# Kernel optimization log

Measured on AMD Instinct MI355X. Metric: run time of the kernel, lower is better.

Reference implementation:

```python
import jax, jax.numpy as jnp
import numpy as np

N_NODES = 100000
N_EDGES = 1600000
N_GRAPHS = 1024
N_FEAT = 128
HID = 64
N_CLASSES = 16
N_CENT = 3  # centroids per class


def setup_inputs() -> dict:
    key = jax.random.key(0)
    ks = jax.random.split(key, 8)
    x = jax.random.normal(ks[0], (N_NODES, N_FEAT), dtype=jnp.float32)
    edge_index = jax.random.randint(ks[1], (2, N_EDGES), 0, N_NODES, dtype=jnp.int64)
    batch = jnp.sort(jax.random.randint(ks[2], (N_NODES,), 0, N_GRAPHS, dtype=jnp.int64))
    s = 1.0 / np.sqrt(N_FEAT)
    W1 = jax.random.normal(ks[3], (N_FEAT, HID), dtype=jnp.float32) * s
    W2 = jax.random.normal(ks[4], (HID, HID), dtype=jnp.float32) * (1.0 / np.sqrt(HID))
    W3 = jax.random.normal(ks[5], (HID, HID), dtype=jnp.float32) * (1.0 / np.sqrt(HID))
    b1 = jnp.zeros((HID,), jnp.float32)
    b2 = jnp.zeros((HID,), jnp.float32)
    b3 = jnp.zeros((HID,), jnp.float32)
    centroids = jax.random.normal(ks[6], (N_CLASSES * N_CENT, HID), dtype=jnp.float32)
    reject_bias = jnp.zeros((1,), jnp.float32)
    return {"x": x, "edge_index": edge_index, "batch": batch,
            "W1": W1, "b1": b1, "W2": W2, "b2": b2, "W3": W3, "b3": b3,
            "centroids": centroids, "reject_bias": reject_bias}


def _gcn_conv(x, W, b, src, dst, norm, n_nodes):
    # PyG GCNConv: out[dst] = sum_e norm_e * (x[src_e] @ W), + bias
    h = x @ W                      # [N, out]
    msg = h[src] * norm[:, None]   # [E+N, out] gather + scale
    out = jax.ops.segment_sum(msg, dst, num_segments=n_nodes)
    return out + b


def reference(x, edge_index, batch, W1, b1, W2, b2, W3, b3, centroids, reject_bias):
    n = x.shape[0]
    loops = jnp.arange(n, dtype=edge_index.dtype)
    src = jnp.concatenate([edge_index[0], loops])
    dst = jnp.concatenate([edge_index[1], loops])
    # symmetric normalization on A + I
    deg = jax.ops.segment_sum(jnp.ones_like(dst, dtype=x.dtype), dst, num_segments=n)
    dinv = jax.lax.rsqrt(jnp.maximum(deg, 1.0))
    norm = dinv[src] * dinv[dst]

    h = jax.nn.relu(_gcn_conv(x, W1, b1, src, dst, norm, n))  # dropout is identity at eval
    h = jax.nn.relu(_gcn_conv(h, W2, b2, src, dst, norm, n))
    h = _gcn_conv(h, W3, b3, src, dst, norm, n)

    # global mean pool over graphs in the batch
    summ = jax.ops.segment_sum(h, batch, num_segments=N_GRAPHS)          # [G, HID]
    cnt = jax.ops.segment_sum(jnp.ones((n,), h.dtype), batch, num_segments=N_GRAPHS)
    emb = summ / jnp.maximum(cnt, 1.0)[:, None]

    # centroid distance head: squared euclidean to all class centroids
    d = (jnp.sum(emb * emb, -1, keepdims=True)
         - 2.0 * emb @ centroids.T
         + jnp.sum(centroids * centroids, -1))                           # [G, 16*3]
    d_pc = jnp.min(d.reshape(-1, N_CLASSES, N_CENT), axis=-1)            # [G, 16]
    class_logits = -d_pc
    reject_logit = jnp.min(d_pc, axis=-1, keepdims=True) - reject_bias   # [G, 1]
    return jnp.concatenate([class_logits, reject_logit], axis=-1)        # [G, 17]
```

## Files before the change

kernel.cpp:

```cpp
#include <hip/hip_runtime.h>

#define HID 64
#define NCLS 16
#define NCENT 3
#define NCENTS (NCLS * NCENT)
#define BSHIFT 9
#define BINW (1 << BSHIFT)
#define NBINMAX 256
#define CHUNK 4096
#define EPT (CHUNK / 256)

static inline int ceil_div(int a, int b) { return (a + b - 1) / b; }

__device__ inline unsigned short f2bf(float f) {
    unsigned int u = __float_as_uint(f);
    return (unsigned short)((u + 0x7FFFu + ((u >> 16) & 1u)) >> 16);
}
__device__ inline float bf2f(unsigned short h) {
    return __uint_as_float(((unsigned int)h) << 16);
}


__global__ void k_count(const int* __restrict__ dst, int* __restrict__ binCnt,
                        int E, int nbins) {
    __shared__ int c[NBINMAX];
    for (int i = threadIdx.x; i < nbins; i += 256) c[i] = 0;
    __syncthreads();
    int e = blockIdx.x * CHUNK + threadIdx.x;
#pragma unroll
    for (int j = 0; j < EPT; j++, e += 256)
        if (e < E) atomicAdd(&c[dst[e] >> BSHIFT], 1);
    __syncthreads();
    for (int i = threadIdx.x; i < nbins; i += 256)
        if (c[i] > 0) atomicAdd(&binCnt[i], c[i]);
}

__global__ void k_binoff(const int* __restrict__ binCnt, int* __restrict__ binBase,
                         int nbins, int E) {
    __shared__ int ts[NBINMAX];
    int t = threadIdx.x;
    int v = (t < nbins) ? binCnt[t] : 0;
    ts[t] = v;
    __syncthreads();
    for (int off = 1; off < NBINMAX; off <<= 1) {
        int x = (t >= off) ? ts[t - off] : 0;
        __syncthreads();
        ts[t] += x;
        __syncthreads();
    }
    if (t < nbins) binBase[t] = ts[t] - v;
    if (t == 0) binBase[nbins] = E;
}

__global__ __launch_bounds__(256) void k_bin(const int* __restrict__ src,
                                             const int* __restrict__ dst,
                                             const int* __restrict__ binBase,
                                             int* __restrict__ binCur,
                                             int2* __restrict__ binned,
                                             int E, int nbins) {
    __shared__ int cnt[NBINMAX], off[NBINMAX], gbase[NBINMAX];
    __shared__ int2 stage[CHUNK];
    const int c0 = blockIdx.x * CHUNK;
    const int tid = threadIdx.x;
    cnt[tid] = 0;
    __syncthreads();
    int sv[EPT], dv[EPT];
#pragma unroll
    for (int j = 0; j < EPT; j++) {
        int e = c0 + j * 256 + tid;
        dv[j] = -1;
        if (e < E) {
            sv[j] = src[e];
            dv[j] = dst[e];
            atomicAdd(&cnt[dv[j] >> BSHIFT], 1);
        }
    }
    __syncthreads();
    off[tid] = cnt[tid];
    __syncthreads();
    for (int o = 1; o < NBINMAX; o <<= 1) {
        int x = (tid >= o) ? off[tid - o] : 0;
        __syncthreads();
        off[tid] += x;
        __syncthreads();
    }
    int excl = off[tid] - cnt[tid];
    __syncthreads();
    off[tid] = excl;
    gbase[tid] = (tid < nbins && cnt[tid] > 0) ? atomicAdd(&binCur[tid], cnt[tid]) : 0;
    cnt[tid] = 0;
    __syncthreads();
#pragma unroll
    for (int j = 0; j < EPT; j++)
        if (dv[j] >= 0) {
            int b = dv[j] >> BSHIFT;
            int pos = off[b] + atomicAdd(&cnt[b], 1);
            stage[pos] = make_int2(sv[j], dv[j]);
        }
    __syncthreads();
    int tot = min(CHUNK, E - c0);
    for (int i = tid; i < tot; i += 256) {
        int2 v = stage[i];
        int b = v.y >> BSHIFT;
        binned[binBase[b] + gbase[b] + (i - off[b])] = v;
    }
}

__global__ __launch_bounds__(256) void k_hist(const int2* __restrict__ binned,
                                              const int* __restrict__ binBase,
                                              int* __restrict__ deg, int N) {
    __shared__ int c[BINW];
    int b = blockIdx.x;
    int s = binBase[b], e = binBase[b + 1];
    int n0 = b << BSHIFT;
    for (int i = threadIdx.x; i < BINW; i += 256) c[i] = 0;
    __syncthreads();
    for (int i = s + threadIdx.x; i < e; i += 256)
        atomicAdd(&c[binned[i].y - n0], 1);
    __syncthreads();
    for (int i = threadIdx.x; i < BINW; i += 256)
        if (n0 + i < N) deg[n0 + i] = c[i];
}


__global__ void k_scan1(const int* __restrict__ deg, int* __restrict__ bsum, int N) {
    __shared__ int ts[256];
    int t = threadIdx.x;
    int base = blockIdx.x * 1024 + t * 4;
    int s = 0;
#pragma unroll
    for (int j = 0; j < 4; j++) if (base + j < N) s += deg[base + j];
    ts[t] = s;
    __syncthreads();
    for (int off = 128; off > 0; off >>= 1) {
        if (t < off) ts[t] += ts[t + off];
        __syncthreads();
    }
    if (t == 0) bsum[blockIdx.x] = ts[0];
}

__global__ void k_scan2(int* __restrict__ bsum, int B) {
    __shared__ int ts[256];
    int t = threadIdx.x;
    int v = (t < B) ? bsum[t] : 0;
    ts[t] = v;
    __syncthreads();
    for (int off = 1; off < 256; off <<= 1) {
        int x = (t >= off) ? ts[t - off] : 0;
        __syncthreads();
        ts[t] += x;
        __syncthreads();
    }
    if (t < B) bsum[t] = ts[t] - v;
}

__global__ void k_scan3(const int* __restrict__ deg, const int* __restrict__ boff,
                        int* __restrict__ rs, float* __restrict__ dinv, int N) {
    __shared__ int ts[256];
    int t = threadIdx.x;
    int base = blockIdx.x * 1024 + t * 4;
    int v[4];
    int s = 0;
#pragma unroll
    for (int j = 0; j < 4; j++) {
        v[j] = (base + j < N) ? deg[base + j] : 0;
        s += v[j];
    }
    ts[t] = s;
    __syncthreads();
    for (int off = 1; off < 256; off <<= 1) {
        int x = (t >= off) ? ts[t - off] : 0;
        __syncthreads();
        ts[t] += x;
        __syncthreads();
    }
    int run = boff[blockIdx.x] + ts[t] - s;
#pragma unroll
    for (int j = 0; j < 4; j++) {
        if (base + j < N) {
            rs[base + j] = run;
            dinv[base + j] = rsqrtf((float)(v[j] + 1));
            run += v[j];
        }
    }
}

__global__ __launch_bounds__(256) void k_fillc(const int2* __restrict__ binned,
                                               const int* __restrict__ binBase,
                                               const int* __restrict__ rs,
                                               int* __restrict__ col, int N) {
    __shared__ int cur[BINW];
    __shared__ int rsl[BINW];
    int b = blockIdx.x;
    int s = binBase[b], e = binBase[b + 1];
    int n0 = b << BSHIFT;
    for (int i = threadIdx.x; i < BINW; i += 256) {
        cur[i] = 0;
        rsl[i] = (n0 + i < N) ? rs[n0 + i] : 0;
    }
    __syncthreads();
    for (int i = s + threadIdx.x; i < e; i += 256) {
        int2 v = binned[i];
        int lo = v.y - n0;
        int pos = rsl[lo] + atomicAdd(&cur[lo], 1);
        col[pos] = v.x;
    }
}


template <int K, bool BF>
__global__ __launch_bounds__(256) void k_gemm(const void* __restrict__ Ain,
                                              const float* __restrict__ W,
                                              unsigned short* __restrict__ out, int N) {
    __shared__ float Ws[64 * HID];
    __shared__ float As[64][68];
    const int tx = threadIdx.x & 15;
    const int ty = threadIdx.x >> 4;
    const int row0 = blockIdx.x * 64;

    float acc[4][4] = {};

    for (int k0 = 0; k0 < K; k0 += 64) {
        if (k0 > 0) __syncthreads();
        for (int i = threadIdx.x; i < 64 * 16; i += 256)
            ((float4*)Ws)[i] = ((const float4*)(W + (size_t)k0 * HID))[i];
        for (int i = threadIdx.x; i < 64 * 16; i += 256) {
            int r = i >> 4, c = i & 15;
            int row = row0 + r;
            float4 v = {0.f, 0.f, 0.f, 0.f};
            if (row < N) {
                if (BF) {
                    ushort4 u = *(const ushort4*)((const unsigned short*)Ain +
                                                  (size_t)row * K + k0 + 4 * c);
                    v.x = bf2f(u.x); v.y = bf2f(u.y); v.z = bf2f(u.z); v.w = bf2f(u.w);
                } else {
                    v = *(const float4*)((const float*)Ain + (size_t)row * K + k0 + 4 * c);
                }
            }
            *(float4*)&As[r][4 * c] = v;
        }
        __syncthreads();
#pragma unroll 4
        for (int k = 0; k < 64; k++) {
            float4 w = *(const float4*)&Ws[k * HID + 4 * tx];
#pragma unroll
            for (int i = 0; i < 4; i++) {
                float a = As[4 * ty + i][k];
                acc[i][0] = fmaf(a, w.x, acc[i][0]);
                acc[i][1] = fmaf(a, w.y, acc[i][1]);
                acc[i][2] = fmaf(a, w.z, acc[i][2]);
                acc[i][3] = fmaf(a, w.w, acc[i][3]);
            }
        }
    }
#pragma unroll
    for (int i = 0; i < 4; i++) {
        int row = row0 + 4 * ty + i;
        if (row < N) {
            ushort4 v = {f2bf(acc[i][0]), f2bf(acc[i][1]), f2bf(acc[i][2]), f2bf(acc[i][3])};
            *(ushort4*)&out[(size_t)row * HID + 4 * tx] = v;
        }
    }
}


__global__ void k_agg(const unsigned short* __restrict__ tin,
                      unsigned short* __restrict__ out,
                      const int* __restrict__ rs, const int* __restrict__ deg,
                      const int* __restrict__ col,
                      const float* __restrict__ dinv, const float* __restrict__ bias,
                      int N, int relu) {
    int node = (blockIdx.x * blockDim.x + threadIdx.x) >> 4;
    int l = threadIdx.x & 15;
    if (node >= N) return;
    float di = dinv[node];
    ushort4 tb = ((const ushort4*)(tin + (size_t)node * HID))[l];
    float s2 = di * di;
    float ax = s2 * bf2f(tb.x), ay = s2 * bf2f(tb.y);
    float az = s2 * bf2f(tb.z), aw = s2 * bf2f(tb.w);

    int beg = rs[node];
    int cnt = deg[node];
    int last = beg + cnt - 1;
    for (int e = 0; e < cnt; e += 8) {
        int sv[8];
#pragma unroll
        for (int j = 0; j < 8; j++) {
            int idx = beg + e + j;
            sv[j] = col[idx < last ? idx : last];
        }
        float dvv[8];
#pragma unroll
        for (int j = 0; j < 8; j++) dvv[j] = dinv[sv[j]];
        ushort4 vv[8];
#pragma unroll
        for (int j = 0; j < 8; j++) vv[j] = ((const ushort4*)(tin + (size_t)sv[j] * HID))[l];
#pragma unroll
        for (int j = 0; j < 8; j++) {
            float w = (e + j < cnt) ? dvv[j] * di : 0.0f;
            ax = fmaf(w, bf2f(vv[j].x), ax); ay = fmaf(w, bf2f(vv[j].y), ay);
            az = fmaf(w, bf2f(vv[j].z), az); aw = fmaf(w, bf2f(vv[j].w), aw);
        }
    }
    float4 b = ((const float4*)bias)[l];
    ax += b.x; ay += b.y; az += b.z; aw += b.w;
    if (relu) {
        ax = fmaxf(ax, 0.f); ay = fmaxf(ay, 0.f);
        az = fmaxf(az, 0.f); aw = fmaxf(aw, 0.f);
    }
    ushort4 o = {f2bf(ax), f2bf(ay), f2bf(az), f2bf(aw)};
    ((ushort4*)(out + (size_t)node * HID))[l] = o;
}


__global__ void k_pool_head(const unsigned short* __restrict__ h,
                            const int* __restrict__ batch,
                            const float* __restrict__ cent, const float* __restrict__ rbias,
                            float* __restrict__ out, int N) {
    int g = blockIdx.x;
    int lo = 0, hi = N;
    while (lo < hi) { int mid = (lo + hi) >> 1; if (batch[mid] < g) lo = mid + 1; else hi = mid; }
    int s = lo;
    lo = 0; hi = N;
    while (lo < hi) { int mid = (lo + hi) >> 1; if (batch[mid] < g + 1) lo = mid + 1; else hi = mid; }
    int e = lo;

    __shared__ float part[4][HID];
    __shared__ float embS[HID];
    __shared__ float dS[NCENTS];
    __shared__ float dpcS[NCLS];

    int lane = threadIdx.x & 63, wid = threadIdx.x >> 6;
    float acc = 0.0f;
    for (int i = s + wid; i < e; i += 4) acc += bf2f(h[(size_t)i * HID + lane]);
    part[wid][lane] = acc;
    __syncthreads();
    if (wid == 0) {
        float v = part[0][lane] + part[1][lane] + part[2][lane] + part[3][lane];
        embS[lane] = v / fmaxf((float)(e - s), 1.0f);
    }
    __syncthreads();
    if (threadIdx.x < NCENTS) {
        const float* c = cent + threadIdx.x * HID;
        float d = 0.0f;
        for (int k = 0; k < HID; k++) { float df = embS[k] - c[k]; d = fmaf(df, df, d); }
        dS[threadIdx.x] = d;
    }
    __syncthreads();
    if (threadIdx.x < NCLS) {
        float m = fminf(dS[threadIdx.x * 3],
                        fminf(dS[threadIdx.x * 3 + 1], dS[threadIdx.x * 3 + 2]));
        dpcS[threadIdx.x] = m;
        out[g * (NCLS + 1) + threadIdx.x] = -m;
    }
    __syncthreads();
    if (threadIdx.x == 0) {
        float m = dpcS[0];
        for (int i = 1; i < NCLS; i++) m = fminf(m, dpcS[i]);
        out[g * (NCLS + 1) + NCLS] = m - rbias[0];
    }
}


extern "C" void kernel_launch(void* const* d_in, const int* in_sizes, int n_in,
                              void* d_out, int out_size, void* d_ws, size_t ws_size,
                              hipStream_t stream) {
    const float* x    = (const float*)d_in[0];
    const int*   ei   = (const int*)d_in[1];
    const int*   bat  = (const int*)d_in[2];
    const float* W1   = (const float*)d_in[3];
    const float* b1   = (const float*)d_in[4];
    const float* W2   = (const float*)d_in[5];
    const float* b2   = (const float*)d_in[6];
    const float* W3   = (const float*)d_in[7];
    const float* b3   = (const float*)d_in[8];
    const float* cent = (const float*)d_in[9];
    const float* rb   = (const float*)d_in[10];
    float* out = (float*)d_out;

    const int N = in_sizes[0] / 128;
    const int E = in_sizes[1] / 2;
    const int B1 = ceil_div(N, 1024);
    const int nbins = (N + BINW - 1) >> BSHIFT;

    char* p = (char*)d_ws;
    unsigned short* A  = (unsigned short*)p; p += (size_t)N * HID * 2;
    unsigned short* Bb = (unsigned short*)p; p += (size_t)N * HID * 2;
    int2*  binned = (int2*)p;  p += (size_t)E * 8;
    int*   col    = (int*)p;   p += (size_t)E * 4;
    float* dinv   = (float*)p; p += (size_t)N * 4;
    int*   rs     = (int*)p;   p += (size_t)N * 4;
    int*   deg    = (int*)p;   p += (size_t)N * 4;
    int*   bsum   = (int*)p;   p += (size_t)((B1 + 1) & ~1) * 4;
    int*   binBase= (int*)p;   p += (NBINMAX + 2) * 4;
    int*   binCnt = (int*)p;   p += NBINMAX * 4;
    int*   binCur = (int*)p;   p += NBINMAX * 4;

    hipMemsetAsync(binCnt, 0, 2 * NBINMAX * 4, stream);

    k_count<<<ceil_div(E, CHUNK), 256, 0, stream>>>(ei + E, binCnt, E, nbins);
    k_binoff<<<1, 256, 0, stream>>>(binCnt, binBase, nbins, E);
    k_bin<<<ceil_div(E, CHUNK), 256, 0, stream>>>(ei, ei + E, binBase, binCur, binned, E, nbins);
    k_hist<<<nbins, 256, 0, stream>>>(binned, binBase, deg, N);
    k_scan1<<<B1, 256, 0, stream>>>(deg, bsum, N);
    k_scan2<<<1, 256, 0, stream>>>(bsum, B1);
    k_scan3<<<B1, 256, 0, stream>>>(deg, bsum, rs, dinv, N);
    k_fillc<<<nbins, 256, 0, stream>>>(binned, binBase, rs, col, N);

    k_gemm<128, false><<<ceil_div(N, 64), 256, 0, stream>>>(x, W1, A, N);
    k_agg<<<ceil_div(N * 16, 256), 256, 0, stream>>>(A, Bb, rs, deg, col, dinv, b1, N, 1);
    k_gemm<64, true><<<ceil_div(N, 64), 256, 0, stream>>>(Bb, W2, A, N);
    k_agg<<<ceil_div(N * 16, 256), 256, 0, stream>>>(A, Bb, rs, deg, col, dinv, b2, N, 1);
    k_gemm<64, true><<<ceil_div(N, 64), 256, 0, stream>>>(Bb, W3, A, N);
    k_agg<<<ceil_div(N * 16, 256), 256, 0, stream>>>(A, Bb, rs, deg, col, dinv, b3, N, 0);

    k_pool_head<<<1024, 256, 0, stream>>>(Bb, bat, cent, rb, out, N);
}
```

Baseline: 364.0 us.

## Fuse CSR histogram, scan and fill into one kernel; widen aggregation lanes

Result: faster. 353.3 us (-2.9%).

```diff
diff --git a/kernel.cpp b/kernel.cpp
--- a/kernel.cpp
+++ b/kernel.cpp
@@ -16,9 +16,14 @@
     unsigned int u = __float_as_uint(f);
     return (unsigned short)((u + 0x7FFFu + ((u >> 16) & 1u)) >> 16);
 }
+__device__ inline unsigned int pack2bf(float lo, float hi) {
+    return (unsigned int)f2bf(lo) | ((unsigned int)f2bf(hi) << 16);
+}
 __device__ inline float bf2f(unsigned short h) {
     return __uint_as_float(((unsigned int)h) << 16);
 }
+__device__ inline float bflo(unsigned int u) { return __uint_as_float(u << 16); }
+__device__ inline float bfhi(unsigned int u) { return __uint_as_float(u & 0xFFFF0000u); }
 
 
 __global__ void k_count(const int* __restrict__ dst, int* __restrict__ binCnt,
@@ -106,44 +111,26 @@
     }
 }
 
-__global__ __launch_bounds__(256) void k_hist(const int2* __restrict__ binned,
-                                              const int* __restrict__ binBase,
-                                              int* __restrict__ deg, int N) {
+__global__ __launch_bounds__(256) void k_fillc2(const int2* __restrict__ binned,
+                                                const int* __restrict__ binBase,
+                                                int* __restrict__ col,
+                                                int* __restrict__ rs_out,
+                                                int* __restrict__ deg_out,
+                                                float* __restrict__ dinv_out, int N) {
     __shared__ int c[BINW];
+    __shared__ int rsl[BINW];
+    __shared__ int ts[256];
     int b = blockIdx.x;
     int s = binBase[b], e = binBase[b + 1];
     int n0 = b << BSHIFT;
-    for (int i = threadIdx.x; i < BINW; i += 256) c[i] = 0;
-    __syncthreads();
-    for (int i = s + threadIdx.x; i < e; i += 256)
+    int t = threadIdx.x;
+    c[2 * t] = 0; c[2 * t + 1] = 0;
+    __syncthreads();
+    for (int i = s + t; i < e; i += 256)
         atomicAdd(&c[binned[i].y - n0], 1);
     __syncthreads();
-    for (int i = threadIdx.x; i < BINW; i += 256)
-        if (n0 + i < N) deg[n0 + i] = c[i];
-}
-
-
-__global__ void k_scan1(const int* __restrict__ deg, int* __restrict__ bsum, int N) {
-    __shared__ int ts[256];
-    int t = threadIdx.x;
-    int base = blockIdx.x * 1024 + t * 4;
-    int s = 0;
-#pragma unroll
-    for (int j = 0; j < 4; j++) if (base + j < N) s += deg[base + j];
-    ts[t] = s;
-    __syncthreads();
-    for (int off = 128; off > 0; off >>= 1) {
-        if (t < off) ts[t] += ts[t + off];
-        __syncthreads();
-    }
-    if (t == 0) bsum[blockIdx.x] = ts[0];
-}
-
-__global__ void k_scan2(int* __restrict__ bsum, int B) {
-    __shared__ int ts[256];
-    int t = threadIdx.x;
-    int v = (t < B) ? bsum[t] : 0;
-    ts[t] = v;
+    int v0 = c[2 * t], v1 = c[2 * t + 1];
+    ts[t] = v0 + v1;
     __syncthreads();
     for (int off = 1; off < 256; off <<= 1) {
         int x = (t >= off) ? ts[t - off] : 0;
@@ -151,58 +138,24 @@
         ts[t] += x;
         __syncthreads();
     }
-    if (t < B) bsum[t] = ts[t] - v;
-}
-
-__global__ void k_scan3(const int* __restrict__ deg, const int* __restrict__ boff,
-                        int* __restrict__ rs, float* __restrict__ dinv, int N) {
-    __shared__ int ts[256];
-    int t = threadIdx.x;
-    int base = blockIdx.x * 1024 + t * 4;
-    int v[4];
-    int s = 0;
-#pragma unroll
-    for (int j = 0; j < 4; j++) {
-        v[j] = (base + j < N) ? deg[base + j] : 0;
-        s += v[j];
-    }
-    ts[t] = s;
-    __syncthreads();
-    for (int off = 1; off < 256; off <<= 1) {
-        int x = (t >= off) ? ts[t - off] : 0;
-        __syncthreads();
-        ts[t] += x;
-        __syncthreads();
-    }
-    int run = boff[blockIdx.x] + ts[t] - s;
-#pragma unroll
-    for (int j = 0; j < 4; j++) {
-        if (base + j < N) {
-            rs[base + j] = run;
-            dinv[base + j] = rsqrtf((float)(v[j] + 1));
-            run += v[j];
-        }
-    }
-}
-
-__global__ __launch_bounds__(256) void k_fillc(const int2* __restrict__ binned,
-                                               const int* __restrict__ binBase,
-                                               const int* __restrict__ rs,
-                                               int* __restrict__ col, int N) {
-    __shared__ int cur[BINW];
-    __shared__ int rsl[BINW];
-    int b = blockIdx.x;
-    int s = binBase[b], e = binBase[b + 1];
-    int n0 = b << BSHIFT;
-    for (int i = threadIdx.x; i < BINW; i += 256) {
-        cur[i] = 0;
-        rsl[i] = (n0 + i < N) ? rs[n0 + i] : 0;
-    }
-    __syncthreads();
-    for (int i = s + threadIdx.x; i < e; i += 256) {
+    int base = binBase[b] + ts[t] - (v0 + v1);
+    rsl[2 * t] = base;
+    rsl[2 * t + 1] = base + v0;
+    int n = n0 + 2 * t;
+    if (n < N) {
+        deg_out[n] = v0; rs_out[n] = base;
+        dinv_out[n] = rsqrtf((float)(v0 + 1));
+    }
+    if (n + 1 < N) {
+        deg_out[n + 1] = v1; rs_out[n + 1] = base + v0;
+        dinv_out[n + 1] = rsqrtf((float)(v1 + 1));
+    }
+    c[2 * t] = 0; c[2 * t + 1] = 0;
+    __syncthreads();
+    for (int i = s + t; i < e; i += 256) {
         int2 v = binned[i];
         int lo = v.y - n0;
-        int pos = rsl[lo] + atomicAdd(&cur[lo], 1);
+        int pos = rsl[lo] + atomicAdd(&c[lo], 1);
         col[pos] = v.x;
     }
 }
@@ -270,14 +223,16 @@
                       const int* __restrict__ col,
                       const float* __restrict__ dinv, const float* __restrict__ bias,
                       int N, int relu) {
-    int node = (blockIdx.x * blockDim.x + threadIdx.x) >> 4;
-    int l = threadIdx.x & 15;
+    int node = (blockIdx.x * blockDim.x + threadIdx.x) >> 3;
+    int l = threadIdx.x & 7;
     if (node >= N) return;
     float di = dinv[node];
-    ushort4 tb = ((const ushort4*)(tin + (size_t)node * HID))[l];
+    uint4 tb = ((const uint4*)(tin + (size_t)node * HID))[l];
     float s2 = di * di;
-    float ax = s2 * bf2f(tb.x), ay = s2 * bf2f(tb.y);
-    float az = s2 * bf2f(tb.z), aw = s2 * bf2f(tb.w);
+    float a0 = s2 * bflo(tb.x), a1 = s2 * bfhi(tb.x);
+    float a2 = s2 * bflo(tb.y), a3 = s2 * bfhi(tb.y);
+    float a4 = s2 * bflo(tb.z), a5 = s2 * bfhi(tb.z);
+    float a6 = s2 * bflo(tb.w), a7 = s2 * bfhi(tb.w);
 
     int beg = rs[node];
     int cnt = deg[node];
@@ -292,24 +247,30 @@
         float dvv[8];
 #pragma unroll
         for (int j = 0; j < 8; j++) dvv[j] = dinv[sv[j]];
-        ushort4 vv[8];
-#pragma unroll
-        for (int j = 0; j < 8; j++) vv[j] = ((const ushort4*)(tin + (size_t)sv[j] * HID))[l];
+        uint4 vv[8];
+#pragma unroll
+        for (int j = 0; j < 8; j++) vv[j] = ((const uint4*)(tin + (size_t)sv[j] * HID))[l];
 #pragma unroll
         for (int j = 0; j < 8; j++) {
             float w = (e + j < cnt) ? dvv[j] * di : 0.0f;
-            ax = fmaf(w, bf2f(vv[j].x), ax); ay = fmaf(w, bf2f(vv[j].y), ay);
-            az = fmaf(w, bf2f(vv[j].z), az); aw = fmaf(w, bf2f(vv[j].w), aw);
-        }
-    }
-    float4 b = ((const float4*)bias)[l];
-    ax += b.x; ay += b.y; az += b.z; aw += b.w;
+            a0 = fmaf(w, bflo(vv[j].x), a0); a1 = fmaf(w, bfhi(vv[j].x), a1);
+            a2 = fmaf(w, bflo(vv[j].y), a2); a3 = fmaf(w, bfhi(vv[j].y), a3);
+            a4 = fmaf(w, bflo(vv[j].z), a4); a5 = fmaf(w, bfhi(vv[j].z), a5);
+            a6 = fmaf(w, bflo(vv[j].w), a6); a7 = fmaf(w, bfhi(vv[j].w), a7);
+        }
+    }
+    float4 b0 = ((const float4*)bias)[2 * l];
+    float4 b1 = ((const float4*)bias)[2 * l + 1];
+    a0 += b0.x; a1 += b0.y; a2 += b0.z; a3 += b0.w;
+    a4 += b1.x; a5 += b1.y; a6 += b1.z; a7 += b1.w;
     if (relu) {
-        ax = fmaxf(ax, 0.f); ay = fmaxf(ay, 0.f);
-        az = fmaxf(az, 0.f); aw = fmaxf(aw, 0.f);
-    }
-    ushort4 o = {f2bf(ax), f2bf(ay), f2bf(az), f2bf(aw)};
-    ((ushort4*)(out + (size_t)node * HID))[l] = o;
+        a0 = fmaxf(a0, 0.f); a1 = fmaxf(a1, 0.f); a2 = fmaxf(a2, 0.f); a3 = fmaxf(a3, 0.f);
+        a4 = fmaxf(a4, 0.f); a5 = fmaxf(a5, 0.f); a6 = fmaxf(a6, 0.f); a7 = fmaxf(a7, 0.f);
+    }
+    uint4 o;
+    o.x = pack2bf(a0, a1); o.y = pack2bf(a2, a3);
+    o.z = pack2bf(a4, a5); o.w = pack2bf(a6, a7);
+    ((uint4*)(out + (size_t)node * HID))[l] = o;
 }
 
 
@@ -380,7 +341,6 @@
 
     const int N = in_sizes[0] / 128;
     const int E = in_sizes[1] / 2;
-    const int B1 = ceil_div(N, 1024);
     const int nbins = (N + BINW - 1) >> BSHIFT;
 
     char* p = (char*)d_ws;
@@ -391,7 +351,6 @@
     float* dinv   = (float*)p; p += (size_t)N * 4;
     int*   rs     = (int*)p;   p += (size_t)N * 4;
     int*   deg    = (int*)p;   p += (size_t)N * 4;
-    int*   bsum   = (int*)p;   p += (size_t)((B1 + 1) & ~1) * 4;
     int*   binBase= (int*)p;   p += (NBINMAX + 2) * 4;
     int*   binCnt = (int*)p;   p += NBINMAX * 4;
     int*   binCur = (int*)p;   p += NBINMAX * 4;
@@ -401,18 +360,14 @@
     k_count<<<ceil_div(E, CHUNK), 256, 0, stream>>>(ei + E, binCnt, E, nbins);
     k_binoff<<<1, 256, 0, stream>>>(binCnt, binBase, nbins, E);
     k_bin<<<ceil_div(E, CHUNK), 256, 0, stream>>>(ei, ei + E, binBase, binCur, binned, E, nbins);
-    k_hist<<<nbins, 256, 0, stream>>>(binned, binBase, deg, N);
-    k_scan1<<<B1, 256, 0, stream>>>(deg, bsum, N);
-    k_scan2<<<1, 256, 0, stream>>>(bsum, B1);
-    k_scan3<<<B1, 256, 0, stream>>>(deg, bsum, rs, dinv, N);
-    k_fillc<<<nbins, 256, 0, stream>>>(binned, binBase, rs, col, N);
+    k_fillc2<<<nbins, 256, 0, stream>>>(binned, binBase, col, rs, deg, dinv, N);
 
     k_gemm<128, false><<<ceil_div(N, 64), 256, 0, stream>>>(x, W1, A, N);
-    k_agg<<<ceil_div(N * 16, 256), 256, 0, stream>>>(A, Bb, rs, deg, col, dinv, b1, N, 1);
+    k_agg<<<ceil_div(N * 8, 256), 256, 0, stream>>>(A, Bb, rs, deg, col, dinv, b1, N, 1);
     k_gemm<64, true><<<ceil_div(N, 64), 256, 0, stream>>>(Bb, W2, A, N);
-    k_agg<<<ceil_div(N * 16, 256), 256, 0, stream>>>(A, Bb, rs, deg, col, dinv, b2, N, 1);
+    k_agg<<<ceil_div(N * 8, 256), 256, 0, stream>>>(A, Bb, rs, deg, col, dinv, b2, N, 1);
     k_gemm<64, true><<<ceil_div(N, 64), 256, 0, stream>>>(Bb, W3, A, N);
-    k_agg<<<ceil_div(N * 16, 256), 256, 0, stream>>>(A, Bb, rs, deg, col, dinv, b3, N, 0);
+    k_agg<<<ceil_div(N * 8, 256), 256, 0, stream>>>(A, Bb, rs, deg, col, dinv, b3, N, 0);
 
     k_pool_head<<<1024, 256, 0, stream>>>(Bb, bat, cent, rb, out, N);
 }
```
